# Kernel optimization log

Measured on AMD Instinct MI355X. Metric: run time of the kernel, lower is better.

Reference implementation:

```python
import jax, jax.numpy as jnp
import numpy as np

N_NODE, N_POD, N_SVC = 500, 20000, 2000
T, F, H, O = 16, 64, 128, 64


def _gconv(x, src, dst, n_dst, W, b):
    # DGL GraphConv, norm='both': out-deg^-1/2 on src, sum-aggregate, in-deg^-1/2 on dst, then linear.
    n_src = x.shape[0]
    outd = jnp.clip(jax.ops.segment_sum(jnp.ones(src.shape, x.dtype), src, num_segments=n_src), 1.0)
    ind = jnp.clip(jax.ops.segment_sum(jnp.ones(dst.shape, x.dtype), dst, num_segments=n_dst), 1.0)
    h = x * jax.lax.rsqrt(outd)[:, None, None]          # [n_src, T, F]
    m = jax.ops.segment_sum(h[src], dst, num_segments=n_dst)  # [n_dst, T, F]
    m = m * jax.lax.rsqrt(ind)[:, None, None]
    return jnp.einsum('ntf,fh->nth', m, W) + b


def _lstm_layer(x, Wih, Whh, bih, bhh):
    # PyTorch LSTM layer, gate order i,f,g,o; x: [B, T, I] batch_first.
    B = x.shape[0]
    Hh = Whh.shape[1]
    def step(carry, xt):
        h, c = carry
        g = xt @ Wih.T + h @ Whh.T + (bih + bhh)
        i, f, gg, o = jnp.split(g, 4, axis=-1)
        c = jax.nn.sigmoid(f) * c + jax.nn.sigmoid(i) * jnp.tanh(gg)
        h = jax.nn.sigmoid(o) * jnp.tanh(c)
        return (h, c), h
    init = (jnp.zeros((B, Hh), x.dtype), jnp.zeros((B, Hh), x.dtype))
    _, hs = jax.lax.scan(step, init, jnp.swapaxes(x, 0, 1))
    return jnp.swapaxes(hs, 0, 1)


def setup_inputs() -> dict:
    key = jax.random.key(0)
    ks = jax.random.split(key, 32)
    p = lambda k, shape, fan: (jax.random.normal(k, shape, jnp.float32) / np.sqrt(fan)).astype(jnp.float32)
    d = {
        'x_node': jax.random.normal(ks[0], (N_NODE, T, F), jnp.float32),
        'x_pod': jax.random.normal(ks[1], (N_POD, T, F), jnp.float32),
        'x_svc': jax.random.normal(ks[2], (N_SVC, T, F), jnp.float32),
        'sc_src': jax.random.randint(ks[3], (16000,), 0, N_SVC),
        'sc_dst': jax.random.randint(ks[4], (16000,), 0, N_SVC),
        'in_src': jax.random.randint(ks[5], (20000,), 0, N_POD),
        'in_dst': jax.random.randint(ks[6], (20000,), 0, N_NODE),
        'ni_src': jax.random.randint(ks[7], (20000,), 0, N_NODE),
        'ni_dst': jax.random.randint(ks[8], (20000,), 0, N_POD),
        'ii_src': jax.random.randint(ks[9], (100000,), 0, N_POD),
        'ii_dst': jax.random.randint(ks[10], (100000,), 0, N_POD),
        'si_src': jax.random.randint(ks[11], (20000,), 0, N_SVC),
        'si_dst': jax.random.randint(ks[12], (20000,), 0, N_POD),
        'is_src': jax.random.randint(ks[13], (20000,), 0, N_POD),
        'is_dst': jax.random.randint(ks[14], (20000,), 0, N_SVC),
        # GraphConv params: weight [in, out], bias [out]
        'W_sc': p(ks[15], (F, H), F), 'b_sc': jnp.zeros((H,), jnp.float32),
        'W_in': p(ks[16], (F, H), F), 'b_in': jnp.zeros((H,), jnp.float32),
        'W_ni': p(ks[17], (F, H), F), 'b_ni': jnp.zeros((H,), jnp.float32),
        'W_ii': p(ks[18], (F, H), F), 'b_ii': jnp.zeros((H,), jnp.float32),
        'W_si': p(ks[19], (F, H), F), 'b_si': jnp.zeros((H,), jnp.float32),
        'W_is': p(ks[20], (F, H), F), 'b_is': jnp.zeros((H,), jnp.float32),
        # 2-layer LSTM params
        'Wih0': p(ks[21], (4 * O, H), H), 'Whh0': p(ks[22], (4 * O, O), O),
        'bih0': jnp.zeros((4 * O,), jnp.float32), 'bhh0': jnp.zeros((4 * O,), jnp.float32),
        'Wih1': p(ks[23], (4 * O, O), O), 'Whh1': p(ks[24], (4 * O, O), O),
        'bih1': jnp.zeros((4 * O,), jnp.float32), 'bhh1': jnp.zeros((4 * O,), jnp.float32),
    }
    return d


def reference(x_node, x_pod, x_svc,
              sc_src, sc_dst, in_src, in_dst, ni_src, ni_dst,
              ii_src, ii_dst, si_src, si_dst, is_src, is_dst,
              W_sc, b_sc, W_in, b_in, W_ni, b_ni, W_ii, b_ii, W_si, b_si, W_is, b_is,
              Wih0, Whh0, bih0, bhh0, Wih1, Whh1, bih1, bhh1):
    # HeteroGraphConv with aggregate='mean' over edge types per dst node type,
    # vectorized over all T timesteps at once (the torch code loops per timestep).
    node = _gconv(x_pod, in_src, in_dst, N_NODE, W_in, b_in)  # only relation into 'node'
    pod = (_gconv(x_node, ni_src, ni_dst, N_POD, W_ni, b_ni)
           + _gconv(x_pod, ii_src, ii_dst, N_POD, W_ii, b_ii)
           + _gconv(x_svc, si_src, si_dst, N_POD, W_si, b_si)) / 3.0
    svc = (_gconv(x_svc, sc_src, sc_dst, N_SVC, W_sc, b_sc)
           + _gconv(x_pod, is_src, is_dst, N_SVC, W_is, b_is)) / 2.0
    feat = jax.nn.relu(jnp.concatenate([node, pod, svc], axis=0))  # [N_total, T, H]
    h = _lstm_layer(feat, Wih0, Whh0, bih0, bhh0)
    h = _lstm_layer(h, Wih1, Whh1, bih1, bhh1)
    return feat, jax.nn.relu(h)
```

## Files before the change

kernel.cpp:

```cpp
#include <hip/hip_runtime.h>

typedef unsigned int u32;

#define N_NODE_ 500
#define N_POD_  20000
#define N_SVC_  2000
#define N_TOT_  22500
#define T_ 16
#define F_ 64
#define H_ 128
#define O_ 64

#define OF_OUTD_SC  0
#define OF_IND_SC   2000
#define OF_OUTD_IN  4000
#define OF_IND_IN   24000
#define OF_OUTD_NI  24500
#define OF_IND_NI   25000
#define OF_OUTD_II  45000
#define OF_IND_II   65000
#define OF_OUTD_SI  85000
#define OF_IND_SI   87000
#define OF_OUTD_IS  107000
#define OF_IND_IS   127000
#define OF_DEG_END  129000
#define OF_W0       129024
#define OF_W1       (129024 + 49152)
#define G_F_SIZE    (129024 + 81920)
#define OI_CNT_IN 0
#define OI_CNT_NI 500
#define OI_CNT_II 20500
#define OI_CNT_SI 40500
#define OI_CNT_SC 60500
#define OI_CNT_IS 62500
#define OI_CNT_END 64500
#define OI_OFF_IN 64500
#define OI_OFF_NI 65001
#define OI_OFF_II 85002
#define OI_OFF_SI 105003
#define OI_OFF_SC 125004
#define OI_OFF_IS 127005
#define OI_CSR_IN 129006
#define OI_CSR_NI 149006
#define OI_CSR_II 169006
#define OI_CSR_SI 269006
#define OI_CSR_SC 289006
#define OI_CSR_IS 305006
#define G_I_SIZE  325006

__device__ __align__(16) float g_f[G_F_SIZE];
__device__ int g_i[G_I_SIZE];

__device__ __forceinline__ float sigf(float x) { return 1.0f / (1.0f + __expf(-x)); }

__device__ __forceinline__ float tanhf_fast(float x) {
  float ax = fabsf(x);
  float e = __expf(2.0f * ax);
  float t = 1.0f - 2.0f / (e + 1.0f);
  return copysignf(t, x);
}

__global__ void zero_k() {
  int i = blockIdx.x * 256 + threadIdx.x;
  if (i < OF_DEG_END + 24) g_f[i] = 0.0f;
  if (i < OI_CNT_END) g_i[i] = 0;
}

struct Rels {
  const int* src[6];
  const int* dst[6];
  int n[6];
  int o_outd[6];
  int o_ind[6];
  int o_cnt[6];
  int o_off[6];
  int o_csr[6];
};

__global__ void deg_all_k(Rels R) {
  int rel = blockIdx.y;
  int e = blockIdx.x * 256 + threadIdx.x;
  if (e < R.n[rel]) {
    atomicAdd(&g_f[R.o_outd[rel] + R.src[rel][e]], 1.0f);
    atomicAdd(&g_f[R.o_ind[rel] + R.dst[rel][e]], 1.0f);
    atomicAdd(&g_i[R.o_cnt[rel] + R.dst[rel][e]], 1);
  }
}

__global__ void fill_all_k(Rels R) {
  int rel = blockIdx.y;
  int e = blockIdx.x * 256 + threadIdx.x;
  if (e < R.n[rel]) {
    int d = R.dst[rel][e];
    int p = atomicAdd(&g_i[R.o_cnt[rel] + d], 1);
    g_i[R.o_csr[rel] + g_i[R.o_off[rel] + d] + p] = R.src[rel][e];
  }
}

__device__ __forceinline__ void tw_one(const float* __restrict__ in, int o_out, int K, int idx) {
  int r = idx / K, k = idx - r * K;
  int q = r >> 6, j = r & 63;
  g_f[o_out + k * 256 + (j << 2) + q] = in[idx];
}

#define PREP2_TOT (OF_DEG_END + 32768 + 16384 + 16384 + 16384)
__global__ void prep2_k(const float* __restrict__ Wih0, const float* __restrict__ Whh0,
                        const float* __restrict__ Wih1, const float* __restrict__ Whh1) {
  int i = blockIdx.x * 256 + threadIdx.x;
  if (i < OF_DEG_END) { g_f[i] = rsqrtf(fmaxf(g_f[i], 1.0f)); return; }
  int j = i - OF_DEG_END;
  if (j < 32768) { tw_one(Wih0, OF_W0, 128, j); return; }
  j -= 32768;
  if (j < 16384) { tw_one(Whh0, OF_W0 + 32768, 64, j); return; }
  j -= 16384;
  if (j < 16384) { tw_one(Wih1, OF_W1, 64, j); return; }
  j -= 16384;
  if (j < 16384) { tw_one(Whh1, OF_W1 + 16384, 64, j); return; }
}

__global__ void exscan6_k() {
  const int cnto[6] = {OI_CNT_IN, OI_CNT_NI, OI_CNT_II, OI_CNT_SI, OI_CNT_SC, OI_CNT_IS};
  const int offo[6] = {OI_OFF_IN, OI_OFF_NI, OI_OFF_II, OI_OFF_SI, OI_OFF_SC, OI_OFF_IS};
  const int ns[6] = {500, 20000, 20000, 20000, 2000, 2000};
  int rel = blockIdx.x;
  int* cnt = g_i + cnto[rel];
  int* off = g_i + offo[rel];
  int n = ns[rel];
  __shared__ int base_s[257];
  __shared__ int part[256];
  int tid = threadIdx.x;
  int chunk = (n + 255) >> 8;
  int lo = tid * chunk;
  int hi = lo + chunk; if (hi > n) hi = n;
  int s = 0;
  for (int i = lo; i < hi; ++i) s += cnt[i];
  part[tid] = s;
  __syncthreads();
  if (tid == 0) {
    int run = 0;
    for (int j = 0; j < 256; ++j) { base_s[j] = run; run += part[j]; }
    base_s[256] = run;
  }
  __syncthreads();
  int run = base_s[tid];
  for (int i = lo; i < hi; ++i) { off[i] = run; run += cnt[i]; cnt[i] = 0; }
  if (tid == 0) off[n] = base_s[256];
}

template <int NREL>
__global__ __launch_bounds__(256) void gconv_gather_k(
    const float* __restrict__ x0, const float* __restrict__ x1, const float* __restrict__ x2,
    int off0, int off1, int off2, int csr0, int csr1, int csr2,
    int od0, int od1, int od2, int id0, int id1, int id2,
    const float* __restrict__ W0, const float* __restrict__ W1, const float* __restrict__ W2,
    const float* __restrict__ b0, const float* __restrict__ b1, const float* __restrict__ b2,
    float scale, float* __restrict__ outp) {
  const float* xs_[3] = {x0, x1, x2};
  const int offs[3] = {off0, off1, off2};
  const int csrs[3] = {csr0, csr1, csr2};
  const int ods[3] = {od0, od1, od2};
  const int ids[3] = {id0, id1, id2};
  const float* Ws[3] = {W0, W1, W2};
  const float* bs[3] = {b0, b1, b2};

  int node = blockIdx.x;
  int tid = threadIdx.x;
  int c = tid & 127;
  int rg = tid >> 7;
  __shared__ float msh[T_][F_];

  float bb = 0.0f;
#pragma unroll
  for (int rel = 0; rel < NREL; ++rel) bb += bs[rel][c];
  float acc[8];
#pragma unroll
  for (int i = 0; i < 8; ++i) acc[i] = bb;

#pragma unroll
  for (int rel = 0; rel < NREL; ++rel) {
    int e0 = g_i[offs[rel] + node], e1 = g_i[offs[rel] + node + 1];
    const int* csr = g_i + csrs[rel];
    const float* od = g_f + ods[rel];
    const float* xr = xs_[rel];
    float a0 = 0.0f, a1 = 0.0f, a2 = 0.0f, a3 = 0.0f;
    for (int e = e0; e < e1; ++e) {
      int s = csr[e];
      float rs = od[s];
      float4 v = ((const float4*)(xr + (size_t)s * 1024))[tid];
      a0 += v.x * rs;
      a1 += v.y * rs;
      a2 += v.z * rs;
      a3 += v.w * rs;
    }
    __syncthreads();
    float* mf = &msh[0][0];
    mf[tid * 4 + 0] = a0;
    mf[tid * 4 + 1] = a1;
    mf[tid * 4 + 2] = a2;
    mf[tid * 4 + 3] = a3;
    __syncthreads();
    float rind = g_f[ids[rel] + node];
    const float* W = Ws[rel];
#pragma unroll 4
    for (int f = 0; f < F_; ++f) {
      float w = W[f * H_ + c] * rind;
#pragma unroll
      for (int i = 0; i < 8; ++i) acc[i] += msh[rg * 8 + i][f] * w;
    }
  }
  float* o = outp + (size_t)node * (T_ * H_);
#pragma unroll
  for (int i = 0; i < 8; ++i) {
    float v = acc[i] * scale;
    o[(rg * 8 + i) * H_ + c] = fmaxf(v, 0.0f);
  }
}

#define RW 6

__device__ __forceinline__ void gemv_lds(float acc[RW][4], const float* xrow0,
                                         const float4* __restrict__ Wb, int nk4, int l) {
#pragma unroll 2
  for (int k4 = 0; k4 < nk4; ++k4) {
    const float4* wp = Wb + (k4 << 8) + l;
    float4 w0 = wp[0];
    float4 w1 = wp[64];
    float4 w2 = wp[128];
    float4 w3 = wp[192];
#pragma unroll
    for (int r = 0; r < RW; ++r) {
      float4 xv = *(const float4*)(xrow0 + r * 256 + k4 * 4);
      acc[r][0] += xv.x * w0.x; acc[r][1] += xv.x * w0.y; acc[r][2] += xv.x * w0.z; acc[r][3] += xv.x * w0.w;
      acc[r][0] += xv.y * w1.x; acc[r][1] += xv.y * w1.y; acc[r][2] += xv.y * w1.z; acc[r][3] += xv.y * w1.w;
      acc[r][0] += xv.z * w2.x; acc[r][1] += xv.z * w2.y; acc[r][2] += xv.z * w2.z; acc[r][3] += xv.z * w2.w;
      acc[r][0] += xv.w * w3.x; acc[r][1] += xv.w * w3.y; acc[r][2] += xv.w * w3.z; acc[r][3] += xv.w * w3.w;
    }
  }
}

__global__ __launch_bounds__(256, 4) void lstm_lds_k(
    const float* __restrict__ feat,
    const float* __restrict__ bih0, const float* __restrict__ bhh0,
    const float* __restrict__ bih1, const float* __restrict__ bhh1,
    float* __restrict__ out2) {
  const float4* W0v = (const float4*)(g_f + OF_W0);
  const float4* W1v = (const float4*)(g_f + OF_W1);
  __shared__ __align__(16) float xh[4][RW][256];
  int tid = threadIdx.x;
  int l = tid & 63;
  int wid = tid >> 6;
  int row0 = (blockIdx.x * 4 + wid) * RW;
  float* xw = &xh[wid][0][0];

  float bb0[4], bb1[4];
#pragma unroll
  for (int q = 0; q < 4; ++q) {
    bb0[q] = bih0[q * 64 + l] + bhh0[q * 64 + l];
    bb1[q] = bih1[q * 64 + l] + bhh1[q * 64 + l];
  }

  const float* xb[RW];
  bool vld[RW];
#pragma unroll
  for (int r = 0; r < RW; ++r) {
    int row = row0 + r;
    vld[r] = row < N_TOT_;
    xb[r] = feat + (size_t)(vld[r] ? row : 0) * (T_ * H_);
  }

  float c0[RW] = {}, c1[RW] = {};
#pragma unroll
  for (int r = 0; r < RW; ++r) {
    xw[r * 256 + 128 + l] = 0.0f;
    xw[r * 256 + 192 + l] = 0.0f;
  }

  float xn0[RW], xn1[RW];
#pragma unroll
  for (int r = 0; r < RW; ++r) {
    xn0[r] = xb[r][l];
    xn1[r] = xb[r][64 + l];
  }

  for (int t = 0; t < T_; ++t) {
#pragma unroll
    for (int r = 0; r < RW; ++r) {
      xw[r * 256 + l] = xn0[r];
      xw[r * 256 + 64 + l] = xn1[r];
    }
    int tn = (t + 1) & 15;
#pragma unroll
    for (int r = 0; r < RW; ++r) {
      xn0[r] = xb[r][tn * H_ + l];
      xn1[r] = xb[r][tn * H_ + 64 + l];
    }

    float acc[RW][4];
#pragma unroll
    for (int r = 0; r < RW; ++r)
#pragma unroll
      for (int q = 0; q < 4; ++q) acc[r][q] = bb0[q];

    gemv_lds(acc, xw, W0v, 48, l);

#pragma unroll
    for (int r = 0; r < RW; ++r) {
      float iv = sigf(acc[r][0]);
      float fv = sigf(acc[r][1]);
      float gv = tanhf_fast(acc[r][2]);
      float ov = sigf(acc[r][3]);
      float cc = fv * c0[r] + iv * gv;
      c0[r] = cc;
      xw[r * 256 + 128 + l] = ov * tanhf_fast(cc);
    }

#pragma unroll
    for (int r = 0; r < RW; ++r)
#pragma unroll
      for (int q = 0; q < 4; ++q) acc[r][q] = bb1[q];

    gemv_lds(acc, xw + 128, W1v, 32, l);

#pragma unroll
    for (int r = 0; r < RW; ++r) {
      float iv = sigf(acc[r][0]);
      float fv = sigf(acc[r][1]);
      float gv = tanhf_fast(acc[r][2]);
      float ov = sigf(acc[r][3]);
      float cc = fv * c1[r] + iv * gv;
      c1[r] = cc;
      float hh = ov * tanhf_fast(cc);
      xw[r * 256 + 192 + l] = hh;
      if (vld[r]) out2[((size_t)(row0 + r) * T_ + t) * O_ + l] = fmaxf(hh, 0.0f);
    }
  }
}

extern "C" void kernel_launch(void* const* d_in, const int* in_sizes, int n_in,
                              void* d_out, int out_size, void* d_ws, size_t ws_size,
                              hipStream_t stream) {
  (void)in_sizes; (void)n_in; (void)out_size; (void)d_ws; (void)ws_size;
  const float* x_node = (const float*)d_in[0];
  const float* x_pod  = (const float*)d_in[1];
  const float* x_svc  = (const float*)d_in[2];
  const int* sc_src = (const int*)d_in[3];
  const int* sc_dst = (const int*)d_in[4];
  const int* in_src = (const int*)d_in[5];
  const int* in_dst = (const int*)d_in[6];
  const int* ni_src = (const int*)d_in[7];
  const int* ni_dst = (const int*)d_in[8];
  const int* ii_src = (const int*)d_in[9];
  const int* ii_dst = (const int*)d_in[10];
  const int* si_src = (const int*)d_in[11];
  const int* si_dst = (const int*)d_in[12];
  const int* is_src = (const int*)d_in[13];
  const int* is_dst = (const int*)d_in[14];
  const float* W_sc = (const float*)d_in[15]; const float* b_sc = (const float*)d_in[16];
  const float* W_in = (const float*)d_in[17]; const float* b_in = (const float*)d_in[18];
  const float* W_ni = (const float*)d_in[19]; const float* b_ni = (const float*)d_in[20];
  const float* W_ii = (const float*)d_in[21]; const float* b_ii = (const float*)d_in[22];
  const float* W_si = (const float*)d_in[23]; const float* b_si = (const float*)d_in[24];
  const float* W_is = (const float*)d_in[25]; const float* b_is = (const float*)d_in[26];
  const float* Wih0 = (const float*)d_in[27]; const float* Whh0 = (const float*)d_in[28];
  const float* bih0 = (const float*)d_in[29]; const float* bhh0 = (const float*)d_in[30];
  const float* Wih1 = (const float*)d_in[31]; const float* Whh1 = (const float*)d_in[32];
  const float* bih1 = (const float*)d_in[33]; const float* bhh1 = (const float*)d_in[34];

  float* out_feat = (float*)d_out;
  float* out_h = out_feat + (size_t)N_TOT_ * T_ * H_;

  Rels R;
  R.src[0] = in_src; R.dst[0] = in_dst; R.n[0] = 20000;
  R.o_outd[0] = OF_OUTD_IN; R.o_ind[0] = OF_IND_IN; R.o_cnt[0] = OI_CNT_IN;
  R.o_off[0] = OI_OFF_IN; R.o_csr[0] = OI_CSR_IN;
  R.src[1] = ni_src; R.dst[1] = ni_dst; R.n[1] = 20000;
  R.o_outd[1] = OF_OUTD_NI; R.o_ind[1] = OF_IND_NI; R.o_cnt[1] = OI_CNT_NI;
  R.o_off[1] = OI_OFF_NI; R.o_csr[1] = OI_CSR_NI;
  R.src[2] = ii_src; R.dst[2] = ii_dst; R.n[2] = 100000;
  R.o_outd[2] = OF_OUTD_II; R.o_ind[2] = OF_IND_II; R.o_cnt[2] = OI_CNT_II;
  R.o_off[2] = OI_OFF_II; R.o_csr[2] = OI_CSR_II;
  R.src[3] = si_src; R.dst[3] = si_dst; R.n[3] = 20000;
  R.o_outd[3] = OF_OUTD_SI; R.o_ind[3] = OF_IND_SI; R.o_cnt[3] = OI_CNT_SI;
  R.o_off[3] = OI_OFF_SI; R.o_csr[3] = OI_CSR_SI;
  R.src[4] = sc_src; R.dst[4] = sc_dst; R.n[4] = 16000;
  R.o_outd[4] = OF_OUTD_SC; R.o_ind[4] = OF_IND_SC; R.o_cnt[4] = OI_CNT_SC;
  R.o_off[4] = OI_OFF_SC; R.o_csr[4] = OI_CSR_SC;
  R.src[5] = is_src; R.dst[5] = is_dst; R.n[5] = 20000;
  R.o_outd[5] = OF_OUTD_IS; R.o_ind[5] = OF_IND_IS; R.o_cnt[5] = OI_CNT_IS;
  R.o_off[5] = OI_OFF_IS; R.o_csr[5] = OI_CSR_IS;

  zero_k<<<(OF_DEG_END + 24 + 255) / 256, 256, 0, stream>>>();

  deg_all_k<<<dim3((100000 + 255) / 256, 6), 256, 0, stream>>>(R);

  prep2_k<<<(PREP2_TOT + 255) / 256, 256, 0, stream>>>(Wih0, Whh0, Wih1, Whh1);

  exscan6_k<<<6, 256, 0, stream>>>();
  fill_all_k<<<dim3((100000 + 255) / 256, 6), 256, 0, stream>>>(R);

  gconv_gather_k<1><<<N_NODE_, 256, 0, stream>>>(
      x_pod, nullptr, nullptr, OI_OFF_IN, 0, 0, OI_CSR_IN, 0, 0,
      OF_OUTD_IN, 0, 0, OF_IND_IN, 0, 0,
      W_in, nullptr, nullptr, b_in, nullptr, nullptr, 1.0f, out_feat);
  gconv_gather_k<3><<<N_POD_, 256, 0, stream>>>(
      x_node, x_pod, x_svc, OI_OFF_NI, OI_OFF_II, OI_OFF_SI, OI_CSR_NI, OI_CSR_II, OI_CSR_SI,
      OF_OUTD_NI, OF_OUTD_II, OF_OUTD_SI, OF_IND_NI, OF_IND_II, OF_IND_SI,
      W_ni, W_ii, W_si, b_ni, b_ii, b_si, 1.0f / 3.0f,
      out_feat + (size_t)N_NODE_ * (T_ * H_));
  gconv_gather_k<2><<<N_SVC_, 256, 0, stream>>>(
      x_svc, x_pod, nullptr, OI_OFF_SC, OI_OFF_IS, 0, OI_CSR_SC, OI_CSR_IS, 0,
      OF_OUTD_SC, OF_OUTD_IS, 0, OF_IND_SC, OF_IND_IS, 0,
      W_sc, W_is, nullptr, b_sc, b_is, nullptr, 0.5f,
      out_feat + (size_t)(N_NODE_ + N_POD_) * (T_ * H_));

  lstm_lds_k<<<1024, 256, 0, stream>>>(
      out_feat, bih0, bhh0, bih1, bhh1, out_h);
}
```

Before: 1.907 ms.

## Stream LSTM weights through double-buffered LDS and raise rows per wave

```diff
diff --git a/kernel.cpp b/kernel.cpp
--- a/kernel.cpp
+++ b/kernel.cpp
@@ -216,20 +216,21 @@
   }
 }
 
-#define RW 6
-
-__device__ __forceinline__ void gemv_lds(float acc[RW][4], const float* xrow0,
-                                         const float4* __restrict__ Wb, int nk4, int l) {
-#pragma unroll 2
-  for (int k4 = 0; k4 < nk4; ++k4) {
-    const float4* wp = Wb + (k4 << 8) + l;
-    float4 w0 = wp[0];
-    float4 w1 = wp[64];
-    float4 w2 = wp[128];
-    float4 w3 = wp[192];
+#define RW 11
+#define NCHT 640
+
+__device__ __forceinline__ void consume8(float acc[RW][4], const float4* __restrict__ wb,
+                                         const float* xbase, int kbase, int l) {
+#pragma unroll
+  for (int kk = 0; kk < 2; ++kk) {
+    float4 w0 = wb[(kk * 4 + 0) * 64 + l];
+    float4 w1 = wb[(kk * 4 + 1) * 64 + l];
+    float4 w2 = wb[(kk * 4 + 2) * 64 + l];
+    float4 w3 = wb[(kk * 4 + 3) * 64 + l];
+    const float* xrp = xbase + kbase + kk * 4;
 #pragma unroll
     for (int r = 0; r < RW; ++r) {
-      float4 xv = *(const float4*)(xrow0 + r * 256 + k4 * 4);
+      float4 xv = *(const float4*)(xrp + r * 256);
       acc[r][0] += xv.x * w0.x; acc[r][1] += xv.x * w0.y; acc[r][2] += xv.x * w0.z; acc[r][3] += xv.x * w0.w;
       acc[r][0] += xv.y * w1.x; acc[r][1] += xv.y * w1.y; acc[r][2] += xv.y * w1.z; acc[r][3] += xv.y * w1.w;
       acc[r][0] += xv.z * w2.x; acc[r][1] += xv.z * w2.y; acc[r][2] += xv.z * w2.z; acc[r][3] += xv.z * w2.w;
@@ -238,14 +239,14 @@
   }
 }
 
-__global__ __launch_bounds__(256, 4) void lstm_lds_k(
+__global__ __launch_bounds__(256, 2) void lstm_wlds_k(
     const float* __restrict__ feat,
     const float* __restrict__ bih0, const float* __restrict__ bhh0,
     const float* __restrict__ bih1, const float* __restrict__ bhh1,
     float* __restrict__ out2) {
-  const float4* W0v = (const float4*)(g_f + OF_W0);
-  const float4* W1v = (const float4*)(g_f + OF_W1);
+  const float4* Wg = (const float4*)(g_f + OF_W0);
   __shared__ __align__(16) float xh[4][RW][256];
+  __shared__ float4 wbuf[2][512];
   int tid = threadIdx.x;
   int l = tid & 63;
   int wid = tid >> 6;
@@ -282,6 +283,34 @@
     xn1[r] = xb[r][64 + l];
   }
 
+  {
+    float4 s0 = Wg[tid], s1 = Wg[256 + tid];
+    wbuf[0][tid] = s0;
+    wbuf[0][tid + 256] = s1;
+  }
+  __syncthreads();
+
+  int gch = 0;
+
+  auto chunk_step = [&](float (&acc)[RW][4], const float* xbase, int kbase) {
+    bool dn = (gch + 1 < NCHT);
+    int noff = ((gch + 1) % 40) << 9;
+    float4 st0, st1;
+    if (dn) {
+      st0 = Wg[noff + tid];
+      st1 = Wg[noff + 256 + tid];
+    }
+    consume8(acc, wbuf[gch & 1], xbase, kbase, l);
+    __syncthreads();
+    if (dn) {
+      float4* wn = wbuf[(gch + 1) & 1];
+      wn[tid] = st0;
+      wn[tid + 256] = st1;
+    }
+    __syncthreads();
+    ++gch;
+  };
+
   for (int t = 0; t < T_; ++t) {
 #pragma unroll
     for (int r = 0; r < RW; ++r) {
@@ -301,7 +330,7 @@
 #pragma unroll
       for (int q = 0; q < 4; ++q) acc[r][q] = bb0[q];
 
-    gemv_lds(acc, xw, W0v, 48, l);
+    for (int cc = 0; cc < 24; ++cc) chunk_step(acc, xw, cc * 8);
 
 #pragma unroll
     for (int r = 0; r < RW; ++r) {
@@ -309,9 +338,9 @@
       float fv = sigf(acc[r][1]);
       float gv = tanhf_fast(acc[r][2]);
       float ov = sigf(acc[r][3]);
-      float cc = fv * c0[r] + iv * gv;
-      c0[r] = cc;
-      xw[r * 256 + 128 + l] = ov * tanhf_fast(cc);
+      float cc_ = fv * c0[r] + iv * gv;
+      c0[r] = cc_;
+      xw[r * 256 + 128 + l] = ov * tanhf_fast(cc_);
     }
 
 #pragma unroll
@@ -319,7 +348,7 @@
 #pragma unroll
       for (int q = 0; q < 4; ++q) acc[r][q] = bb1[q];
 
-    gemv_lds(acc, xw + 128, W1v, 32, l);
+    for (int cc = 0; cc < 16; ++cc) chunk_step(acc, xw + 128, cc * 8);
 
 #pragma unroll
     for (int r = 0; r < RW; ++r) {
@@ -327,9 +356,9 @@
       float fv = sigf(acc[r][1]);
       float gv = tanhf_fast(acc[r][2]);
       float ov = sigf(acc[r][3]);
-      float cc = fv * c1[r] + iv * gv;
-      c1[r] = cc;
-      float hh = ov * tanhf_fast(cc);
+      float cc_ = fv * c1[r] + iv * gv;
+      c1[r] = cc_;
+      float hh = ov * tanhf_fast(cc_);
       xw[r * 256 + 192 + l] = hh;
       if (vld[r]) out2[((size_t)(row0 + r) * T_ + t) * O_ + l] = fmaxf(hh, 0.0f);
     }
@@ -413,6 +442,6 @@
       W_sc, W_is, nullptr, b_sc, b_is, nullptr, 0.5f,
       out_feat + (size_t)(N_NODE_ + N_POD_) * (T_ * H_));
 
-  lstm_lds_k<<<1024, 256, 0, stream>>>(
+  lstm_wlds_k<<<512, 256, 0, stream>>>(
       out_feat, bih0, bhh0, bih1, bhh1, out_h);
 }
```

New measurement: 1.756 ms. -7.9%, faster.

## Use packed FP32 FMA in LSTM GEMV and raise rows per wave to eleven

Applied to the files above, without the earlier changes.

```diff
diff --git a/kernel.cpp b/kernel.cpp
--- a/kernel.cpp
+++ b/kernel.cpp
@@ -1,6 +1,8 @@
 #include <hip/hip_runtime.h>
 
 typedef unsigned int u32;
+typedef float f32x2 __attribute__((ext_vector_type(2)));
+typedef float f32x4 __attribute__((ext_vector_type(4)));
 
 #define N_NODE_ 500
 #define N_POD_  20000
@@ -60,6 +62,15 @@
   return copysignf(t, x);
 }
 
+__device__ __forceinline__ void pk_lo(f32x2& a, f32x2 x, f32x2 w) {
+  asm("v_pk_fma_f32 %0, %1, %2, %0 op_sel:[0,0,0] op_sel_hi:[0,1,1]"
+      : "+v"(a) : "v"(x), "v"(w));
+}
+__device__ __forceinline__ void pk_hi(f32x2& a, f32x2 x, f32x2 w) {
+  asm("v_pk_fma_f32 %0, %1, %2, %0 op_sel:[1,0,0] op_sel_hi:[1,1,1]"
+      : "+v"(a) : "v"(x), "v"(w));
+}
+
 __global__ void zero_k() {
   int i = blockIdx.x * 256 + threadIdx.x;
   if (i < OF_DEG_END + 24) g_f[i] = 0.0f;
@@ -216,35 +227,38 @@
   }
 }
 
-#define RW 6
-
-__device__ __forceinline__ void gemv_lds(float acc[RW][4], const float* xrow0,
-                                         const float4* __restrict__ Wb, int nk4, int l) {
+#define RW 11
+
+__device__ __forceinline__ void gemv_pk(f32x2 accA[RW], f32x2 accB[RW], const float* xrow0,
+                                        const f32x4* __restrict__ Wb, int nk4, int l) {
 #pragma unroll 2
   for (int k4 = 0; k4 < nk4; ++k4) {
-    const float4* wp = Wb + (k4 << 8) + l;
-    float4 w0 = wp[0];
-    float4 w1 = wp[64];
-    float4 w2 = wp[128];
-    float4 w3 = wp[192];
+    const f32x4* wp = Wb + (k4 << 8) + l;
+    f32x4 w0 = wp[0], w1 = wp[64], w2 = wp[128], w3 = wp[192];
+    f32x2 w0A = __builtin_shufflevector(w0, w0, 0, 1), w0B = __builtin_shufflevector(w0, w0, 2, 3);
+    f32x2 w1A = __builtin_shufflevector(w1, w1, 0, 1), w1B = __builtin_shufflevector(w1, w1, 2, 3);
+    f32x2 w2A = __builtin_shufflevector(w2, w2, 0, 1), w2B = __builtin_shufflevector(w2, w2, 2, 3);
+    f32x2 w3A = __builtin_shufflevector(w3, w3, 0, 1), w3B = __builtin_shufflevector(w3, w3, 2, 3);
 #pragma unroll
     for (int r = 0; r < RW; ++r) {
-      float4 xv = *(const float4*)(xrow0 + r * 256 + k4 * 4);
-      acc[r][0] += xv.x * w0.x; acc[r][1] += xv.x * w0.y; acc[r][2] += xv.x * w0.z; acc[r][3] += xv.x * w0.w;
-      acc[r][0] += xv.y * w1.x; acc[r][1] += xv.y * w1.y; acc[r][2] += xv.y * w1.z; acc[r][3] += xv.y * w1.w;
-      acc[r][0] += xv.z * w2.x; acc[r][1] += xv.z * w2.y; acc[r][2] += xv.z * w2.z; acc[r][3] += xv.z * w2.w;
-      acc[r][0] += xv.w * w3.x; acc[r][1] += xv.w * w3.y; acc[r][2] += xv.w * w3.z; acc[r][3] += xv.w * w3.w;
-    }
-  }
-}
-
-__global__ __launch_bounds__(256, 4) void lstm_lds_k(
+      f32x4 xv = *(const f32x4*)(xrow0 + r * 256 + k4 * 4);
+      f32x2 xp0 = __builtin_shufflevector(xv, xv, 0, 1);
+      f32x2 xp1 = __builtin_shufflevector(xv, xv, 2, 3);
+      pk_lo(accA[r], xp0, w0A); pk_lo(accB[r], xp0, w0B);
+      pk_hi(accA[r], xp0, w1A); pk_hi(accB[r], xp0, w1B);
+      pk_lo(accA[r], xp1, w2A); pk_lo(accB[r], xp1, w2B);
+      pk_hi(accA[r], xp1, w3A); pk_hi(accB[r], xp1, w3B);
+    }
+  }
+}
+
+__global__ __launch_bounds__(256, 2) void lstm_pk_k(
     const float* __restrict__ feat,
     const float* __restrict__ bih0, const float* __restrict__ bhh0,
     const float* __restrict__ bih1, const float* __restrict__ bhh1,
     float* __restrict__ out2) {
-  const float4* W0v = (const float4*)(g_f + OF_W0);
-  const float4* W1v = (const float4*)(g_f + OF_W1);
+  const f32x4* W0v = (const f32x4*)(g_f + OF_W0);
+  const f32x4* W1v = (const f32x4*)(g_f + OF_W1);
   __shared__ __align__(16) float xh[4][RW][256];
   int tid = threadIdx.x;
   int l = tid & 63;
@@ -252,12 +266,10 @@
   int row0 = (blockIdx.x * 4 + wid) * RW;
   float* xw = &xh[wid][0][0];
 
-  float bb0[4], bb1[4];
-#pragma unroll
-  for (int q = 0; q < 4; ++q) {
-    bb0[q] = bih0[q * 64 + l] + bhh0[q * 64 + l];
-    bb1[q] = bih1[q * 64 + l] + bhh1[q * 64 + l];
-  }
+  f32x2 bbA0 = {bih0[l] + bhh0[l], bih0[64 + l] + bhh0[64 + l]};
+  f32x2 bbB0 = {bih0[128 + l] + bhh0[128 + l], bih0[192 + l] + bhh0[192 + l]};
+  f32x2 bbA1 = {bih1[l] + bhh1[l], bih1[64 + l] + bhh1[64 + l]};
+  f32x2 bbB1 = {bih1[128 + l] + bhh1[128 + l], bih1[192 + l] + bhh1[192 + l]};
 
   const float* xb[RW];
   bool vld[RW];
@@ -295,38 +307,34 @@
       xn1[r] = xb[r][tn * H_ + 64 + l];
     }
 
-    float acc[RW][4];
-#pragma unroll
-    for (int r = 0; r < RW; ++r)
-#pragma unroll
-      for (int q = 0; q < 4; ++q) acc[r][q] = bb0[q];
-
-    gemv_lds(acc, xw, W0v, 48, l);
+    f32x2 accA[RW], accB[RW];
+#pragma unroll
+    for (int r = 0; r < RW; ++r) { accA[r] = bbA0; accB[r] = bbB0; }
+
+    gemv_pk(accA, accB, xw, W0v, 48, l);
 
 #pragma unroll
     for (int r = 0; r < RW; ++r) {
-      float iv = sigf(acc[r][0]);
-      float fv = sigf(acc[r][1]);
-      float gv = tanhf_fast(acc[r][2]);
-      float ov = sigf(acc[r][3]);
+      float iv = sigf(accA[r][0]);
+      float fv = sigf(accA[r][1]);
+      float gv = tanhf_fast(accB[r][0]);
+      float ov = sigf(accB[r][1]);
       float cc = fv * c0[r] + iv * gv;
       c0[r] = cc;
       xw[r * 256 + 128 + l] = ov * tanhf_fast(cc);
     }
 
 #pragma unroll
-    for (int r = 0; r < RW; ++r)
-#pragma unroll
-      for (int q = 0; q < 4; ++q) acc[r][q] = bb1[q];
-
-    gemv_lds(acc, xw + 128, W1v, 32, l);
+    for (int r = 0; r < RW; ++r) { accA[r] = bbA1; accB[r] = bbB1; }
+
+    gemv_pk(accA, accB, xw + 128, W1v, 32, l);
 
 #pragma unroll
     for (int r = 0; r < RW; ++r) {
-      float iv = sigf(acc[r][0]);
-      float fv = sigf(acc[r][1]);
-      float gv = tanhf_fast(acc[r][2]);
-      float ov = sigf(acc[r][3]);
+      float iv = sigf(accA[r][0]);
+      float fv = sigf(accA[r][1]);
+      float gv = tanhf_fast(accB[r][0]);
+      float ov = sigf(accB[r][1]);
       float cc = fv * c1[r] + iv * gv;
       c1[r] = cc;
       float hh = ov * tanhf_fast(cc);
@@ -413,6 +421,6 @@
       W_sc, W_is, nullptr, b_sc, b_is, nullptr, 0.5f,
       out_feat + (size_t)(N_NODE_ + N_POD_) * (T_ * H_));
 
-  lstm_lds_k<<<1024, 256, 0, stream>>>(
+  lstm_pk_k<<<512, 256, 0, stream>>>(
       out_feat, bih0, bhh0, bih1, bhh1, out_h);
 }
```

New measurement: 1.767 ms. 7.3% less time.
